# Optimization experiments

Measured on AMD Instinct MI355X. Metric: run time of the kernel, lower is better.

## Reference

```python
import jax, jax.numpy as jnp
import numpy as np

T, BS, N, D_IN, D_OUT, H_FFN = 256, 64, 128, 64, 16, 64


def setup_inputs() -> dict:
    key = jax.random.key(0)
    ks = jax.random.split(key, 12)
    s = 1.0 / float(np.sqrt(D_IN))
    uni = lambda k, shp: jax.random.uniform(k, shp, jnp.float32, -s, s)
    return {
        "u": jax.random.normal(ks[0], (T, BS, D_IN), jnp.float32),
        "y": jax.random.normal(ks[1], (T, BS, D_OUT), jnp.float32),
        "W_ih": uni(ks[2], (D_IN, D_IN)),
        "W_hh": uni(ks[3], (D_IN, D_IN)),
        "b_ih": uni(ks[4], (D_IN,)),
        "b_hh": uni(ks[5], (D_IN,)),
        "W1": uni(ks[6], (D_IN, H_FFN)),
        "b1": uni(ks[7], (H_FFN,)),
        "W2": uni(ks[8], (H_FFN, D_OUT)),
        "b2": uni(ks[9], (D_OUT,)),
        # sigma matrices are diag(abs(rand(dim))) in torch; keep the diagonal vector
        "sigma_x_diag": jax.random.uniform(ks[10], (D_IN,), jnp.float32, 0.05, 1.0),
        "sigma_y_diag": jax.random.uniform(ks[11], (D_OUT,), jnp.float32, 0.05, 1.0),
    }


def reference(u, y, W_ih, W_hh, b_ih, b_hh, W1, b1, W2, b2, sigma_x_diag, sigma_y_diag):
    bs = u.shape[1]
    base = jax.random.key(42)
    # x0 = torch.randn(bs, N, input_size)
    x0 = jax.random.normal(jax.random.fold_in(base, 2**20), (bs, N, D_IN), jnp.float32)
    # MVN .sample() is detached from sigma params in torch
    std_x = jax.lax.stop_gradient(jnp.sqrt(sigma_x_diag))
    std_y = jax.lax.stop_gradient(jnp.sqrt(sigma_y_diag))
    sig_y = jax.lax.stop_gradient(sigma_y_diag)
    LOG2PI = jnp.log(jnp.asarray(2.0 * np.pi, jnp.float32))

    def ffn(x):
        return jax.nn.relu(x @ W1 + b1) @ W2 + b2

    def step(x, inp):
        u_k, y_k, t = inp
        k = jax.random.fold_in(base, t)
        k1, k2, k3 = jax.random.split(k, 3)
        # RNNCell(tanh); u_k broadcast over the particle dim (repeat_interleave in torch)
        x = jnp.tanh(u_k[:, None, :] @ W_ih + b_ih + x @ W_hh + b_hh)  # [bs,N,D_IN]
        x = x + std_x * jax.random.normal(k1, x.shape, x.dtype)        # eta noise
        x = jax.lax.stop_gradient(x)                                    # fisher: x.detach()
        y_hat = ffn(x) + std_y * jax.random.normal(k2, (bs, N, D_OUT), x.dtype)  # eps noise
        # log N(y_hat; y_k, diag(sigma_y)), fully detached (torch uses .detach())
        d = jax.lax.stop_gradient(y_hat) - y_k[:, None, :]
        logw = (-0.5 * jnp.sum(d * d / sig_y, axis=-1)
                - 0.5 * jnp.sum(jnp.log(sig_y)) - 0.5 * D_OUT * LOG2PI)  # [bs,N]
        # softmax + multinomial(w, N, replacement=True) == categorical on logits
        I = jax.random.categorical(k3, logw, axis=-1, shape=(N, bs)).T   # [bs,N]
        x = jnp.take_along_axis(x, I[:, :, None], axis=1)                # resample
        return x, y_hat

    ts = jnp.arange(u.shape[0], dtype=jnp.int32)
    _, preds = jax.lax.scan(step, x0, (u, y, ts))
    return preds  # [T, bs, N, D_OUT]
```

## Files before the change

### kernel.cpp

```cpp
#include <hip/hip_runtime.h>
#include <stdint.h>

#define TB 512

__device__ __forceinline__ uint32_t rotl32(uint32_t v, int s) {
    return (v << s) | (v >> (32 - s));
}

__device__ __forceinline__ void threefry2x32(uint32_t k0, uint32_t k1,
                                             uint32_t c0, uint32_t c1,
                                             uint32_t& o0, uint32_t& o1) {
    const uint32_t ks2 = k0 ^ k1 ^ 0x1BD11BDAu;
    uint32_t x0 = c0 + k0;
    uint32_t x1 = c1 + k1;
    x0 += x1; x1 = rotl32(x1, 13); x1 ^= x0;
    x0 += x1; x1 = rotl32(x1, 15); x1 ^= x0;
    x0 += x1; x1 = rotl32(x1, 26); x1 ^= x0;
    x0 += x1; x1 = rotl32(x1, 6);  x1 ^= x0;
    x0 += k1;  x1 += ks2 + 1u;
    x0 += x1; x1 = rotl32(x1, 17); x1 ^= x0;
    x0 += x1; x1 = rotl32(x1, 29); x1 ^= x0;
    x0 += x1; x1 = rotl32(x1, 16); x1 ^= x0;
    x0 += x1; x1 = rotl32(x1, 24); x1 ^= x0;
    x0 += ks2; x1 += k0 + 2u;
    x0 += x1; x1 = rotl32(x1, 13); x1 ^= x0;
    x0 += x1; x1 = rotl32(x1, 15); x1 ^= x0;
    x0 += x1; x1 = rotl32(x1, 26); x1 ^= x0;
    x0 += x1; x1 = rotl32(x1, 6);  x1 ^= x0;
    x0 += k0;  x1 += k1 + 3u;
    x0 += x1; x1 = rotl32(x1, 17); x1 ^= x0;
    x0 += x1; x1 = rotl32(x1, 29); x1 ^= x0;
    x0 += x1; x1 = rotl32(x1, 16); x1 ^= x0;
    x0 += x1; x1 = rotl32(x1, 24); x1 ^= x0;
    x0 += k1;  x1 += ks2 + 4u;
    x0 += x1; x1 = rotl32(x1, 13); x1 ^= x0;
    x0 += x1; x1 = rotl32(x1, 15); x1 ^= x0;
    x0 += x1; x1 = rotl32(x1, 26); x1 ^= x0;
    x0 += x1; x1 = rotl32(x1, 6);  x1 ^= x0;
    x0 += ks2; x1 += k0 + 5u;
    o0 = x0; o1 = x1;
}

__device__ __forceinline__ uint32_t jax_random_bits(uint32_t k0, uint32_t k1, uint32_t i) {
    uint32_t o0, o1;
    threefry2x32(k0, k1, 0u, i, o0, o1);
    return o0 ^ o1;
}

__device__ __forceinline__ float erfinv_f32(float x) {
    float w = -log1pf(-x * x);
    float p;
    if (w < 5.0f) {
        w = w - 2.5f;
        p = 2.81022636e-08f;
        p = fmaf(p, w, 3.43273939e-07f);
        p = fmaf(p, w, -3.5233877e-06f);
        p = fmaf(p, w, -4.39150654e-06f);
        p = fmaf(p, w, 0.00021858087f);
        p = fmaf(p, w, -0.00125372503f);
        p = fmaf(p, w, -0.00417768164f);
        p = fmaf(p, w, 0.246640727f);
        p = fmaf(p, w, 1.50140941f);
    } else {
        w = sqrtf(w) - 3.0f;
        p = -0.000200214257f;
        p = fmaf(p, w, 0.000100950558f);
        p = fmaf(p, w, 0.00134934322f);
        p = fmaf(p, w, -0.00367342844f);
        p = fmaf(p, w, 0.00573950773f);
        p = fmaf(p, w, -0.0076224613f);
        p = fmaf(p, w, 0.00943887047f);
        p = fmaf(p, w, 1.00167406f);
        p = fmaf(p, w, 2.83297682f);
    }
    return p * x;
}

__device__ __forceinline__ float normal_from_bits(uint32_t bits) {
    float f = __uint_as_float((bits >> 9) | 0x3F800000u) - 1.0f;
    float uu = fmaxf(-0.99999994f, fmaf(f, 2.0f, -0.99999994f));
    return 1.41421354f * erfinv_f32(uu);
}

__device__ __forceinline__ float gumbel_from_bits(uint32_t bits) {
    float f = __uint_as_float((bits >> 9) | 0x3F800000u) - 1.0f;
    float uu = fmaxf(1.17549435e-38f, f + 1.17549435e-38f);
    return -logf(-logf(uu));
}

__device__ __forceinline__ float jax_normal_elem(uint32_t k0, uint32_t k1, uint32_t i) {
    return normal_from_bits(jax_random_bits(k0, k1, i));
}

__device__ __forceinline__ void step_keys(int t, uint32_t& kx0, uint32_t& kx1,
                                          uint32_t& ky0, uint32_t& ky1,
                                          uint32_t& kc0, uint32_t& kc1) {
    uint32_t kk0, kk1;
    threefry2x32(0u, 42u, 0u, (uint32_t)t, kk0, kk1);
    threefry2x32(kk0, kk1, 0u, 0u, kx0, kx1);
    threefry2x32(kk0, kk1, 0u, 1u, ky0, ky1);
    threefry2x32(kk0, kk1, 0u, 2u, kc0, kc1);
}

constexpr size_t CONS_OFF  = 0;
constexpr size_t READY_OFF = 256;
constexpr size_t RING_OFF  = 65792;
constexpr int SLOT_FULL_F = 26688;
constexpr int XNZ_O = 0, ONZ_O = 8192, GUM_O = 10240, UBP_O = 26624;

__global__ __launch_bounds__(TB, 2) void smc_pc(
    const float* __restrict__ u, const float* __restrict__ y,
    const float* __restrict__ W_ih, const float* __restrict__ W_hh,
    const float* __restrict__ b_ih, const float* __restrict__ b_hh,
    const float* __restrict__ W1, const float* __restrict__ b1,
    const float* __restrict__ W2, const float* __restrict__ b2,
    const float* __restrict__ sigx, const float* __restrict__ sigy,
    float* __restrict__ out, float* __restrict__ ring,
    uint32_t* __restrict__ ready, uint32_t* __restrict__ cons, int R) {
    const int bid = blockIdx.x;
    const int tid = threadIdx.x;
    const int b = bid & 63;

    if (bid >= 64) {
        const int k = (bid >> 6) - 1;
        for (int t = k; t < 256; t += 3) {
            if (t >= R) {
                if (tid == 0) {
                    while ((int)__hip_atomic_load(&cons[b], __ATOMIC_ACQUIRE,
                                                  __HIP_MEMORY_SCOPE_AGENT) < t - R + 1)
                        __builtin_amdgcn_s_sleep(8);
                }
                __syncthreads();
            }
            uint32_t kx0, kx1, ky0, ky1, kc0, kc1;
            step_keys(t, kx0, kx1, ky0, ky1, kc0, kc1);
            float* slot = ring + ((size_t)b * R + (size_t)(t % R)) * (size_t)SLOT_FULL_F;
            for (int it = tid; it < 8192; it += TB)
                slot[XNZ_O + it] = jax_normal_elem(kx0, kx1, (uint32_t)(b * 8192 + it));
            for (int it = tid; it < 2048; it += TB)
                slot[ONZ_O + it] = jax_normal_elem(ky0, ky1, (uint32_t)(b * 2048 + it));
            for (int it = tid; it < 16384; it += TB)
                slot[GUM_O + it] = gumbel_from_bits(jax_random_bits(
                    kc0, kc1, ((uint32_t)(it >> 7) << 13) + (uint32_t)b * 128u + (uint32_t)(it & 127)));
            if (tid < 64) {
                const float* ut = u + ((size_t)t * 64 + b) * 64;
                float s = 0.f;
                #pragma unroll 4
                for (int k2 = 0; k2 < 64; ++k2) s = fmaf(ut[k2], W_ih[k2 * 64 + tid], s);
                slot[UBP_O + tid] = s + b_ih[tid];
            }
            __threadfence();
            __syncthreads();
            if (tid == 0)
                __hip_atomic_store(&ready[b * 256 + t], 1u, __ATOMIC_RELEASE,
                                   __HIP_MEMORY_SCOPE_AGENT);
        }
        return;
    }

    __shared__ __align__(16) float S0[128][68];
    __shared__ __align__(16) float S1[128][68];
    __shared__ __align__(16) float Whh[64][68];
    __shared__ __align__(16) float W1s[64][68];
    __shared__ __align__(16) float W2s[64][16];
    __shared__ float logw[128];
    __shared__ float bhhs[64], b1s[64], b2s[16], stdxv[64], stdyv[16], sigyv[16], ykv[16];
    __shared__ int   anc[128];

    for (int i = tid; i < 4096; i += TB) {
        const int r = i >> 6, c = i & 63;
        Whh[r][c] = W_hh[i];
        W1s[r][c] = W1[i];
    }
    for (int i = tid; i < 1024; i += TB) W2s[i >> 4][i & 15] = W2[i];
    if (tid < 64) { bhhs[tid] = b_hh[tid]; b1s[tid] = b1[tid]; stdxv[tid] = sqrtf(sigx[tid]); }
    if (tid < 16) { b2s[tid] = b2[tid]; sigyv[tid] = sigy[tid]; stdyv[tid] = sqrtf(sigy[tid]); }
    if (tid < 128) anc[tid] = tid;

    {
        uint32_t xk0, xk1;
        threefry2x32(0u, 42u, 0u, 1048576u, xk0, xk1);
        for (int it = tid; it < 8192; it += TB) {
            const uint32_t idx = (uint32_t)b * 8192u + (uint32_t)it;
            S0[it >> 6][it & 63] = jax_normal_elem(xk0, xk1, idx);
        }
    }
    __syncthreads();

    for (int t = 0; t < 256; ++t) {
        if (tid == 0) {
            if (!__hip_atomic_load(&ready[b * 256 + t], __ATOMIC_RELAXED,
                                   __HIP_MEMORY_SCOPE_AGENT)) {
                while (!__hip_atomic_load(&ready[b * 256 + t], __ATOMIC_RELAXED,
                                          __HIP_MEMORY_SCOPE_AGENT))
                    __builtin_amdgcn_s_sleep(2);
            }
            (void)__hip_atomic_load(&ready[b * 256 + t], __ATOMIC_ACQUIRE,
                                    __HIP_MEMORY_SCOPE_AGENT);
        }
        __syncthreads();
        const float* slot = ring + ((size_t)b * R + (size_t)(t % R)) * (size_t)SLOT_FULL_F;
        float (*Srd)[68] = (t & 1) ? S1 : S0;
        float (*Swr)[68] = (t & 1) ? S0 : S1;
        const float* yt = y + ((size_t)t * 64 + b) * 16;

        {
            if (tid < 16) ykv[tid] = yt[tid];
            const int n0 = (tid >> 4) << 2;
            const int d0 = (tid & 15) << 2;
            int ar[4];
            #pragma unroll
            for (int i = 0; i < 4; ++i) ar[i] = anc[n0 + i];
            float4 ub4 = *(const float4*)(slot + UBP_O + d0);
            float4 z[4];
            #pragma unroll
            for (int i = 0; i < 4; ++i)
                z[i] = *(const float4*)&slot[XNZ_O + (n0 + i) * 64 + d0];
            float acc[4][4];
            #pragma unroll
            for (int i = 0; i < 4; ++i)
                #pragma unroll
                for (int j = 0; j < 4; ++j) acc[i][j] = 0.f;
            #pragma unroll 4
            for (int k4 = 0; k4 < 64; k4 += 4) {
                float4 a[4];
                #pragma unroll
                for (int i = 0; i < 4; ++i) a[i] = *(const float4*)&Srd[ar[i]][k4];
                #pragma unroll
                for (int kk = 0; kk < 4; ++kk) {
                    const float4 wr = *(const float4*)&Whh[k4 + kk][d0];
                    #pragma unroll
                    for (int i = 0; i < 4; ++i) {
                        const float av = (&a[i].x)[kk];
                        acc[i][0] = fmaf(av, wr.x, acc[i][0]);
                        acc[i][1] = fmaf(av, wr.y, acc[i][1]);
                        acc[i][2] = fmaf(av, wr.z, acc[i][2]);
                        acc[i][3] = fmaf(av, wr.w, acc[i][3]);
                    }
                }
            }
            #pragma unroll
            for (int i = 0; i < 4; ++i) {
                float4 res;
                #pragma unroll
                for (int j = 0; j < 4; ++j) {
                    const float v = tanhf(((&ub4.x)[j] + acc[i][j]) + bhhs[d0 + j]);
                    (&res.x)[j] = v + stdxv[d0 + j] * (&z[i].x)[j];
                }
                *(float4*)&Swr[n0 + i][d0] = res;
            }
        }
        __syncthreads();

        {
            const int n0 = (tid >> 4) << 2;
            const int d0 = (tid & 15) << 2;
            float acc[4][4];
            #pragma unroll
            for (int i = 0; i < 4; ++i)
                #pragma unroll
                for (int j = 0; j < 4; ++j) acc[i][j] = 0.f;
            #pragma unroll 4
            for (int k4 = 0; k4 < 64; k4 += 4) {
                float4 a[4];
                #pragma unroll
                for (int i = 0; i < 4; ++i) a[i] = *(const float4*)&Swr[n0 + i][k4];
                #pragma unroll
                for (int kk = 0; kk < 4; ++kk) {
                    const float4 wr = *(const float4*)&W1s[k4 + kk][d0];
                    #pragma unroll
                    for (int i = 0; i < 4; ++i) {
                        const float av = (&a[i].x)[kk];
                        acc[i][0] = fmaf(av, wr.x, acc[i][0]);
                        acc[i][1] = fmaf(av, wr.y, acc[i][1]);
                        acc[i][2] = fmaf(av, wr.z, acc[i][2]);
                        acc[i][3] = fmaf(av, wr.w, acc[i][3]);
                    }
                }
            }
            #pragma unroll
            for (int i = 0; i < 4; ++i) {
                float4 res;
                #pragma unroll
                for (int j = 0; j < 4; ++j)
                    (&res.x)[j] = fmaxf(acc[i][j] + b1s[d0 + j], 0.0f);
                *(float4*)&Srd[n0 + i][d0] = res;
            }
        }
        __syncthreads();

        {
            const int n = tid >> 2;
            const int d0 = (tid & 3) << 2;
            float4 acc = make_float4(0.f, 0.f, 0.f, 0.f);
            #pragma unroll 4
            for (int j4 = 0; j4 < 64; j4 += 4) {
                const float4 h4 = *(const float4*)&Srd[n][j4];
                #pragma unroll
                for (int jj = 0; jj < 4; ++jj) {
                    const float4 wr = *(const float4*)&W2s[j4 + jj][d0];
                    const float hv = (&h4.x)[jj];
                    acc.x = fmaf(hv, wr.x, acc.x);
                    acc.y = fmaf(hv, wr.y, acc.y);
                    acc.z = fmaf(hv, wr.z, acc.z);
                    acc.w = fmaf(hv, wr.w, acc.w);
                }
            }
            const float4 z4 = *(const float4*)&slot[ONZ_O + n * 16 + d0];
            float4 res;
            float s = 0.f;
            #pragma unroll
            for (int j = 0; j < 4; ++j) {
                const int d = d0 + j;
                const float yhv = ((&acc.x)[j] + b2s[d]) + stdyv[d] * (&z4.x)[j];
                (&res.x)[j] = yhv;
                const float dd = yhv - ykv[d];
                s += (dd * dd) / sigyv[d];
            }
            *(float4*)&out[(((size_t)t * 64 + b) * 128 + n) * 16 + d0] = res;
            const float s1 = __shfl_down(s, 1);
            const float s2 = __shfl_down(s, 2);
            const float s3 = __shfl_down(s, 3);
            if ((tid & 3) == 0) logw[n] = -0.5f * (((s + s1) + s2) + s3);
        }
        __syncthreads();

        {
            const int p = tid >> 2;
            const int sub = tid & 3;
            const float* gp = slot + GUM_O + p * 128 + (sub << 5);
            float best = -3.402823466e+38f;
            int bi = 0;
            for (int m4 = 0; m4 < 32; m4 += 4) {
                const float4 g4 = *(const float4*)&gp[m4];
                #pragma unroll
                for (int j = 0; j < 4; ++j) {
                    const int n = (sub << 5) + m4 + j;
                    const float v = logw[n] + (&g4.x)[j];
                    if (v > best) { best = v; bi = n; }
                }
            }
            #pragma unroll
            for (int off = 1; off < 4; off <<= 1) {
                const float ov = __shfl_xor(best, off);
                const int   oi = __shfl_xor(bi, off);
                if (ov > best || (ov == best && oi < bi)) { best = ov; bi = oi; }
            }
            if (sub == 0) anc[p] = bi;
        }
        __syncthreads();

        if (tid == 0)
            __hip_atomic_store(&cons[b], (uint32_t)(t + 1), __ATOMIC_RELEASE,
                               __HIP_MEMORY_SCOPE_AGENT);
    }
}

__global__ __launch_bounds__(TB, 2) void smc_mono(
    const float* __restrict__ u, const float* __restrict__ y,
    const float* __restrict__ W_ih, const float* __restrict__ W_hh,
    const float* __restrict__ b_ih, const float* __restrict__ b_hh,
    const float* __restrict__ W1, const float* __restrict__ b1,
    const float* __restrict__ W2, const float* __restrict__ b2,
    const float* __restrict__ sigx, const float* __restrict__ sigy,
    float* __restrict__ out) {
    const int b = blockIdx.x;
    const int tid = threadIdx.x;

    __shared__ __align__(16) float xs[128][68];
    __shared__ __align__(16) float xn[128][68];
    __shared__ __align__(16) float Wihs[64][68];
    __shared__ __align__(16) float Whh[64][68];
    __shared__ __align__(16) float W1s[64][68];
    __shared__ __align__(16) float W2s[64][16];
    __shared__ __align__(16) float yh[128][16];
    __shared__ float logw[128];
    __shared__ float ubp[64];
    __shared__ float bhhs[64], b1s[64], b2s[16], stdxv[64], stdyv[16], sigyv[16], ykv[16];
    __shared__ int   anc[128];

    for (int i = tid; i < 4096; i += TB) {
        const int r = i >> 6, c = i & 63;
        Wihs[r][c] = W_ih[i];
        Whh[r][c]  = W_hh[i];
        W1s[r][c]  = W1[i];
    }
    for (int i = tid; i < 1024; i += TB) W2s[i >> 4][i & 15] = W2[i];
    if (tid < 64) { bhhs[tid] = b_hh[tid]; b1s[tid] = b1[tid]; stdxv[tid] = sqrtf(sigx[tid]); }
    if (tid < 16) { b2s[tid] = b2[tid]; sigyv[tid] = sigy[tid]; stdyv[tid] = sqrtf(sigy[tid]); }

    {
        uint32_t xk0, xk1;
        threefry2x32(0u, 42u, 0u, 1048576u, xk0, xk1);
        for (int it = tid; it < 8192; it += TB) {
            const uint32_t idx = (uint32_t)b * 8192u + (uint32_t)it;
            xs[it >> 6][it & 63] = jax_normal_elem(xk0, xk1, idx);
        }
    }
    __syncthreads();

    for (int t = 0; t < 256; ++t) {
        uint32_t kx0, kx1, ky0, ky1, kc0, kc1;
        step_keys(t, kx0, kx1, ky0, ky1, kc0, kc1);

        const float* ut = u + ((size_t)t * 64 + b) * 64;
        const float* yt = y + ((size_t)t * 64 + b) * 16;
        if (tid < 64) {
            float s = 0.f;
            #pragma unroll 4
            for (int k = 0; k < 64; ++k) s = fmaf(ut[k], Wihs[k][tid], s);
            ubp[tid] = s + b_ih[tid];
        }
        if (tid < 16) ykv[tid] = yt[tid];
        __syncthreads();

        {
            const int n0 = (tid >> 4) * 4;
            const int d0 = (tid & 15) * 4;
            float acc[4][4];
            #pragma unroll
            for (int i = 0; i < 4; ++i)
                #pragma unroll
                for (int j = 0; j < 4; ++j) acc[i][j] = 0.f;
            #pragma unroll 4
            for (int k4 = 0; k4 < 64; k4 += 4) {
                float4 a[4];
                #pragma unroll
                for (int i = 0; i < 4; ++i) a[i] = *(const float4*)&xs[n0 + i][k4];
                #pragma unroll
                for (int kk = 0; kk < 4; ++kk) {
                    const float4 wr = *(const float4*)&Whh[k4 + kk][d0];
                    #pragma unroll
                    for (int i = 0; i < 4; ++i) {
                        const float av = (&a[i].x)[kk];
                        acc[i][0] = fmaf(av, wr.x, acc[i][0]);
                        acc[i][1] = fmaf(av, wr.y, acc[i][1]);
                        acc[i][2] = fmaf(av, wr.z, acc[i][2]);
                        acc[i][3] = fmaf(av, wr.w, acc[i][3]);
                    }
                }
            }
            #pragma unroll
            for (int i = 0; i < 4; ++i) {
                const int n = n0 + i;
                float4 res;
                #pragma unroll
                for (int j = 0; j < 4; ++j) {
                    const int d = d0 + j;
                    (&res.x)[j] = tanhf((ubp[d] + acc[i][j]) + bhhs[d]);
                }
                *(float4*)&xn[n][d0] = res;
            }
            #pragma unroll
            for (int i = 0; i < 4; ++i) {
                const int n = n0 + i;
                float4 v = *(const float4*)&xn[n][d0];
                #pragma unroll
                for (int j = 0; j < 4; ++j) {
                    const int d = d0 + j;
                    const uint32_t idx = (uint32_t)(b * 8192 + n * 64 + d);
                    (&v.x)[j] = (&v.x)[j] + stdxv[d] * jax_normal_elem(kx0, kx1, idx);
                }
                *(float4*)&xn[n][d0] = v;
            }
        }
        __syncthreads();

        {
            const int n0 = (tid >> 4) * 4;
            const int d0 = (tid & 15) * 4;
            float acc[4][4];
            #pragma unroll
            for (int i = 0; i < 4; ++i)
                #pragma unroll
                for (int j = 0; j < 4; ++j) acc[i][j] = 0.f;
            #pragma unroll 4
            for (int k4 = 0; k4 < 64; k4 += 4) {
                float4 a[4];
                #pragma unroll
                for (int i = 0; i < 4; ++i) a[i] = *(const float4*)&xn[n0 + i][k4];
                #pragma unroll
                for (int kk = 0; kk < 4; ++kk) {
                    const float4 wr = *(const float4*)&W1s[k4 + kk][d0];
                    #pragma unroll
                    for (int i = 0; i < 4; ++i) {
                        const float av = (&a[i].x)[kk];
                        acc[i][0] = fmaf(av, wr.x, acc[i][0]);
                        acc[i][1] = fmaf(av, wr.y, acc[i][1]);
                        acc[i][2] = fmaf(av, wr.z, acc[i][2]);
                        acc[i][3] = fmaf(av, wr.w, acc[i][3]);
                    }
                }
            }
            #pragma unroll
            for (int i = 0; i < 4; ++i) {
                float4 res;
                #pragma unroll
                for (int j = 0; j < 4; ++j)
                    (&res.x)[j] = fmaxf(acc[i][j] + b1s[d0 + j], 0.0f);
                *(float4*)&xs[n0 + i][d0] = res;
            }
        }
        __syncthreads();

        {
            const int n = tid >> 2;
            const int d0 = (tid & 3) * 4;
            float4 acc = make_float4(0.f, 0.f, 0.f, 0.f);
            #pragma unroll 4
            for (int j4 = 0; j4 < 64; j4 += 4) {
                const float4 h4 = *(const float4*)&xs[n][j4];
                #pragma unroll
                for (int jj = 0; jj < 4; ++jj) {
                    const float4 wr = *(const float4*)&W2s[j4 + jj][d0];
                    const float hv = (&h4.x)[jj];
                    acc.x = fmaf(hv, wr.x, acc.x);
                    acc.y = fmaf(hv, wr.y, acc.y);
                    acc.z = fmaf(hv, wr.z, acc.z);
                    acc.w = fmaf(hv, wr.w, acc.w);
                }
            }
            float4 res;
            #pragma unroll
            for (int j = 0; j < 4; ++j) {
                const int d = d0 + j;
                const float v = (&acc.x)[j] + b2s[d];
                const float nz = jax_normal_elem(ky0, ky1, (uint32_t)(b * 2048 + n * 16 + d));
                const float yhv = v + stdyv[d] * nz;
                yh[n][d] = yhv;
                (&res.x)[j] = yhv;
            }
            *(float4*)&out[(((size_t)t * 64 + b) * 128 + n) * 16 + d0] = res;
        }
        __syncthreads();

        if (tid < 128) {
            float s = 0.f;
            for (int d = 0; d < 16; ++d) {
                const float dd = yh[tid][d] - ykv[d];
                s += (dd * dd) / sigyv[d];
            }
            logw[tid] = -0.5f * s;
        }
        __syncthreads();

        {
            const int p = tid >> 2;
            const int sub = tid & 3;
            float best = -3.402823466e+38f;
            int bi = 0;
            const uint32_t base_idx = (uint32_t)p * 8192u + (uint32_t)b * 128u;
            for (int m = 0; m < 32; ++m) {
                const int n = (sub << 5) + m;
                const float v = logw[n] + gumbel_from_bits(jax_random_bits(kc0, kc1, base_idx + (uint32_t)n));
                if (v > best) { best = v; bi = n; }
            }
            #pragma unroll
            for (int off = 1; off < 4; off <<= 1) {
                const float ov = __shfl_xor(best, off);
                const int   oi = __shfl_xor(bi, off);
                if (ov > best || (ov == best && oi < bi)) { best = ov; bi = oi; }
            }
            if (sub == 0) anc[p] = bi;
        }
        __syncthreads();

        for (int it = tid; it < 2048; it += TB) {
            const int n = it >> 4, qq = (it & 15) * 4;
            *(float4*)&xs[n][qq] = *(const float4*)&xn[anc[n]][qq];
        }
        __syncthreads();
    }
}

extern "C" void kernel_launch(void* const* d_in, const int* in_sizes, int n_in,
                              void* d_out, int out_size, void* d_ws, size_t ws_size,
                              hipStream_t stream) {
    const float* u    = (const float*)d_in[0];
    const float* y    = (const float*)d_in[1];
    const float* W_ih = (const float*)d_in[2];
    const float* W_hh = (const float*)d_in[3];
    const float* b_ih = (const float*)d_in[4];
    const float* b_hh = (const float*)d_in[5];
    const float* W1   = (const float*)d_in[6];
    const float* b1   = (const float*)d_in[7];
    const float* W2   = (const float*)d_in[8];
    const float* b2   = (const float*)d_in[9];
    const float* sigx = (const float*)d_in[10];
    const float* sigy = (const float*)d_in[11];
    float* out = (float*)d_out;

    const size_t needF3 = RING_OFF + (size_t)64 * 3 * SLOT_FULL_F * 4;
    const size_t needF2 = RING_OFF + (size_t)64 * 2 * SLOT_FULL_F * 4;
    int R = 0;
    if (ws_size >= needF3)      R = 3;
    else if (ws_size >= needF2) R = 2;

    if (R > 0) {
        uint32_t* cons  = (uint32_t*)((char*)d_ws + CONS_OFF);
        uint32_t* ready = (uint32_t*)((char*)d_ws + READY_OFF);
        float*    ring  = (float*)((char*)d_ws + RING_OFF);
        hipMemsetAsync(d_ws, 0, RING_OFF, stream);
        void* args[] = {
            (void*)&u, (void*)&y, (void*)&W_ih, (void*)&W_hh, (void*)&b_ih,
            (void*)&b_hh, (void*)&W1, (void*)&b1, (void*)&W2, (void*)&b2,
            (void*)&sigx, (void*)&sigy, (void*)&out, (void*)&ring,
            (void*)&ready, (void*)&cons, (void*)&R};
        hipLaunchCooperativeKernel((const void*)smc_pc, dim3(256), dim3(TB),
                                   args, 0, stream);
    } else {
        hipLaunchKernelGGL(smc_mono, dim3(64), dim3(TB), 0, stream,
                           u, y, W_ih, W_hh, b_ih, b_hh, W1, b1, W2, b2, sigx, sigy, out);
    }
}
```

Baseline: 7.944 ms.

## Pass resample ancestors via wavefront shuffles and drop per-step block barriers

Ancestor indices now stay in registers and are passed with wavefront shuffles instead of a shared-memory array. This removes the end-of-step barrier. Every thread now polls the producer's ready flag itself, which removes the barrier after the tid-0 spin. The consumer progress counter is also published earlier in the step, so the producer can refill ring slots sooner. The cost is more global atomic polling traffic from all threads, and a greater risk of subtle ordering bugs from the barriers that were removed.

```diff
diff --git a/kernel.cpp b/kernel.cpp
--- a/kernel.cpp
+++ b/kernel.cpp
@@ -165,7 +165,12 @@
     __shared__ __align__(16) float W2s[64][16];
     __shared__ float logw[128];
     __shared__ float bhhs[64], b1s[64], b2s[16], stdxv[64], stdyv[16], sigyv[16], ykv[16];
-    __shared__ int   anc[128];
+
+    const int n0p = (tid >> 4) << 2;
+    const int d0p = (tid & 15) << 2;
+    int ar[4];
+    #pragma unroll
+    for (int i = 0; i < 4; ++i) ar[i] = n0p + i;
 
     for (int i = tid; i < 4096; i += TB) {
         const int r = i >> 6, c = i & 63;
@@ -175,7 +180,6 @@
     for (int i = tid; i < 1024; i += TB) W2s[i >> 4][i & 15] = W2[i];
     if (tid < 64) { bhhs[tid] = b_hh[tid]; b1s[tid] = b1[tid]; stdxv[tid] = sqrtf(sigx[tid]); }
     if (tid < 16) { b2s[tid] = b2[tid]; sigyv[tid] = sigy[tid]; stdyv[tid] = sqrtf(sigy[tid]); }
-    if (tid < 128) anc[tid] = tid;
 
     {
         uint32_t xk0, xk1;
@@ -188,7 +192,8 @@
     __syncthreads();
 
     for (int t = 0; t < 256; ++t) {
-        if (tid == 0) {
+        {
+            volatile uint32_t* rf = &ready[b * 256 + t];
             if (!__hip_atomic_load(&ready[b * 256 + t], __ATOMIC_RELAXED,
                                    __HIP_MEMORY_SCOPE_AGENT)) {
                 while (!__hip_atomic_load(&ready[b * 256 + t], __ATOMIC_RELAXED,
@@ -197,8 +202,8 @@
             }
             (void)__hip_atomic_load(&ready[b * 256 + t], __ATOMIC_ACQUIRE,
                                     __HIP_MEMORY_SCOPE_AGENT);
-        }
-        __syncthreads();
+            (void)rf;
+        }
         const float* slot = ring + ((size_t)b * R + (size_t)(t % R)) * (size_t)SLOT_FULL_F;
         float (*Srd)[68] = (t & 1) ? S1 : S0;
         float (*Swr)[68] = (t & 1) ? S0 : S1;
@@ -206,16 +211,11 @@
 
         {
             if (tid < 16) ykv[tid] = yt[tid];
-            const int n0 = (tid >> 4) << 2;
-            const int d0 = (tid & 15) << 2;
-            int ar[4];
-            #pragma unroll
-            for (int i = 0; i < 4; ++i) ar[i] = anc[n0 + i];
-            float4 ub4 = *(const float4*)(slot + UBP_O + d0);
+            float4 ub4 = *(const float4*)(slot + UBP_O + d0p);
             float4 z[4];
             #pragma unroll
             for (int i = 0; i < 4; ++i)
-                z[i] = *(const float4*)&slot[XNZ_O + (n0 + i) * 64 + d0];
+                z[i] = *(const float4*)&slot[XNZ_O + (n0p + i) * 64 + d0p];
             float acc[4][4];
             #pragma unroll
             for (int i = 0; i < 4; ++i)
@@ -228,7 +228,7 @@
                 for (int i = 0; i < 4; ++i) a[i] = *(const float4*)&Srd[ar[i]][k4];
                 #pragma unroll
                 for (int kk = 0; kk < 4; ++kk) {
-                    const float4 wr = *(const float4*)&Whh[k4 + kk][d0];
+                    const float4 wr = *(const float4*)&Whh[k4 + kk][d0p];
                     #pragma unroll
                     for (int i = 0; i < 4; ++i) {
                         const float av = (&a[i].x)[kk];
@@ -244,17 +244,18 @@
                 float4 res;
                 #pragma unroll
                 for (int j = 0; j < 4; ++j) {
-                    const float v = tanhf(((&ub4.x)[j] + acc[i][j]) + bhhs[d0 + j]);
-                    (&res.x)[j] = v + stdxv[d0 + j] * (&z[i].x)[j];
-                }
-                *(float4*)&Swr[n0 + i][d0] = res;
-            }
-        }
-        __syncthreads();
-
-        {
-            const int n0 = (tid >> 4) << 2;
-            const int d0 = (tid & 15) << 2;
+                    const float v = tanhf(((&ub4.x)[j] + acc[i][j]) + bhhs[d0p + j]);
+                    (&res.x)[j] = v + stdxv[d0p + j] * (&z[i].x)[j];
+                }
+                *(float4*)&Swr[n0p + i][d0p] = res;
+            }
+        }
+        __syncthreads();
+        if (tid == 0)
+            __hip_atomic_store(&cons[b], (uint32_t)t, __ATOMIC_RELEASE,
+                               __HIP_MEMORY_SCOPE_AGENT);
+
+        {
             float acc[4][4];
             #pragma unroll
             for (int i = 0; i < 4; ++i)
@@ -264,10 +265,10 @@
             for (int k4 = 0; k4 < 64; k4 += 4) {
                 float4 a[4];
                 #pragma unroll
-                for (int i = 0; i < 4; ++i) a[i] = *(const float4*)&Swr[n0 + i][k4];
+                for (int i = 0; i < 4; ++i) a[i] = *(const float4*)&Swr[n0p + i][k4];
                 #pragma unroll
                 for (int kk = 0; kk < 4; ++kk) {
-                    const float4 wr = *(const float4*)&W1s[k4 + kk][d0];
+                    const float4 wr = *(const float4*)&W1s[k4 + kk][d0p];
                     #pragma unroll
                     for (int i = 0; i < 4; ++i) {
                         const float av = (&a[i].x)[kk];
@@ -283,8 +284,8 @@
                 float4 res;
                 #pragma unroll
                 for (int j = 0; j < 4; ++j)
-                    (&res.x)[j] = fmaxf(acc[i][j] + b1s[d0 + j], 0.0f);
-                *(float4*)&Srd[n0 + i][d0] = res;
+                    (&res.x)[j] = fmaxf(acc[i][j] + b1s[d0p + j], 0.0f);
+                *(float4*)&Srd[n0p + i][d0p] = res;
             }
         }
         __syncthreads();
@@ -346,13 +347,10 @@
                 const int   oi = __shfl_xor(bi, off);
                 if (ov > best || (ov == best && oi < bi)) { best = ov; bi = oi; }
             }
-            if (sub == 0) anc[p] = bi;
-        }
-        __syncthreads();
-
-        if (tid == 0)
-            __hip_atomic_store(&cons[b], (uint32_t)(t + 1), __ATOMIC_RELEASE,
-                               __HIP_MEMORY_SCOPE_AGENT);
+            #pragma unroll
+            for (int i = 0; i < 4; ++i)
+                ar[i] = __shfl(bi, ((n0p + i) << 2) & 63);
+        }
     }
 }
 
```

Measured after the change: 10.31 ms. 1.3x slower.
